# Kernel tuning notes

Measured on AMD Instinct MI355X. Metric: run time of the kernel, lower is better.

## Reference

```python
import jax, jax.numpy as jnp
import numpy as np

B, LAT, H, K = 8, 128, 1024, 294
N, E = 100000, 1600000
XSIZE = 128.0
TAU = 0.5
STEPS = 3


def setup_inputs() -> dict:
    key = jax.random.key(0)
    ks = jax.random.split(key, 20)
    s_in = 1.0 / np.sqrt(LAT)
    s_h = 1.0 / np.sqrt(H)
    inp = {
        "latent": jax.random.normal(ks[0], (B, LAT), jnp.float32),
        "W0": jax.random.normal(ks[1], (LAT, H), jnp.float32) * s_in,
        "b0": jnp.zeros((H,), jnp.float32),
        "W1": jax.random.normal(ks[2], (H, H), jnp.float32) * s_h,
        "b1": jnp.zeros((H,), jnp.float32),
        "W2": jax.random.normal(ks[3], (H, H), jnp.float32) * s_h,
        "b2": jnp.zeros((H,), jnp.float32),
        "W3": jax.random.normal(ks[4], (H, H), jnp.float32) * s_h,
        "b3": jnp.zeros((H,), jnp.float32),
        # coefficient heads use normal(1e-4) init in the source
        "Wx": jax.random.normal(ks[5], (H, K), jnp.float32) * 1e-4,
        "bx": jnp.zeros((K,), jnp.float32),
        "Wy": jax.random.normal(ks[6], (H, K), jnp.float32) * 1e-4,
        "by": jnp.zeros((K,), jnp.float32),
        "Wz": jax.random.normal(ks[7], (H, K), jnp.float32) * 1e-4,
        "bz": jnp.zeros((K,), jnp.float32),
        # precomputed Zernike/spherical basis evaluated at the N coords: [K, N]
        "Z": jax.random.normal(ks[8], (K, N), jnp.float32),
        "edge_weights": jax.random.uniform(ks[9], (E,), jnp.float32),
        "edge_index": jax.random.randint(ks[10], (2, E), 0, N, jnp.int64),
    }
    return inp


def _decode_coefficients(latent, W0, b0, W1, b1, W2, b2, W3, b3,
                         Wx, bx, Wy, by, Wz, bz):
    h = jax.nn.relu(latent @ W0 + b0)
    for W, b in ((W1, b1), (W2, b2), (W3, b3)):
        h = jax.nn.relu(h + h @ W + b)  # residual MLP block
    return h @ Wx + bx, h @ Wy + by, h @ Wz + bz  # [B, K] each


def _diffuse(flow, edge_index, edge_weights):
    """Graph diffusion smoothing of per-node vectors. flow: [B, N, 3]."""
    src, dst = edge_index[0], edge_index[1]
    deg = jax.ops.segment_sum(edge_weights, dst, num_segments=N)
    deg = jnp.maximum(deg, 1e-6)[:, None, None]  # [N,1,1]
    f = jnp.transpose(flow, (1, 0, 2))  # [N, B, 3]
    w = edge_weights[:, None, None]
    for _ in range(STEPS):
        msg = f[src] * w                                        # gather  [E,B,3]
        agg = jax.ops.segment_sum(msg, dst, num_segments=N)     # scatter [N,B,3]
        f = (1.0 - TAU) * f + TAU * agg / deg
    return jnp.transpose(f, (1, 0, 2))  # [B, N, 3]


def reference(latent, W0, b0, W1, b1, W2, b2, W3, b3,
              Wx, bx, Wy, by, Wz, bz, Z, edge_weights, edge_index):
    cx, cy, cz = _decode_coefficients(latent, W0, b0, W1, b1, W2, b2, W3, b3,
                                      Wx, bx, Wy, by, Wz, bz)
    # basis evaluation: per-axis coefficients contracted with Zernike basis
    dx = jnp.einsum("bk,kn->bn", cx, Z)
    dy = jnp.einsum("bk,kn->bn", cy, Z)
    dz = jnp.einsum("bk,kn->bn", cz, Z)
    flow = (0.5 * XSIZE) * jnp.stack([dx, dy, dz], axis=-1)  # [B, N, 3]
    flow = _diffuse(flow, edge_index, edge_weights)
    reg = 1e-4 * jnp.sqrt(jnp.sum(cx ** 2 + cy ** 2 + cz ** 2))
    return flow, reg
```

## Files before the change

### kernel.cpp

```cpp
#include <hip/hip_runtime.h>
#include <math.h>

#define BB 8
#define LAT 128
#define HH 1024
#define KK 294
#define NN 100000
#define EE 1600000
#define NSTEPS 3
#define XS_HALF 64.0f

#define NB 391
#define CS 8
#define COB 28
#define COB2 30
#define EPT 8
#define EST 200000
#define EBLK 782
#define GON 40

#define F2NB 782
#define KPAD 320
#define GS 80

__constant__ float ccoefT[KPAD * 24];


__device__ __forceinline__ void mlp_part_body(int bid, const float* __restrict__ hin,
                                              const float* __restrict__ W,
                                              float* __restrict__ part, int jdim) {
    int it = bid & 15;
    int bs = bid >> 4;
    int tx = threadIdx.x;
    int il = tx & 63;
    int jg = tx >> 6;
    int i = it * 64 + il;
    int j0 = bs * 64;

    __shared__ float hs[8 * 64];
    for (int u = tx; u < 512; u += 256) {
        int b = u >> 6, lj = u & 63;
        hs[u] = hin[b * jdim + j0 + lj];
    }
    __syncthreads();

    float acc[8];
#pragma unroll
    for (int b = 0; b < 8; ++b) acc[b] = 0.0f;
#pragma unroll
    for (int jj = 0; jj < 16; ++jj) {
        int lj = jg * 16 + jj;
        float w = W[(size_t)(j0 + lj) * HH + i];
#pragma unroll
        for (int b = 0; b < 8; ++b) acc[b] += hs[b * 64 + lj] * w;
    }

    __shared__ float red[4][8][64];
#pragma unroll
    for (int b = 0; b < 8; ++b) red[jg][b][il] = acc[b];
    __syncthreads();
    for (int u = tx; u < 512; u += 256) {
        int b = u >> 6, ii = u & 63;
        float s = red[0][b][ii] + red[1][b][ii] + red[2][b][ii] + red[3][b][ii];
        part[(size_t)bs * 8192 + b * HH + it * 64 + ii] = s;
    }
}

__device__ __forceinline__ void mlp_comb_body(int bid, const float* __restrict__ part,
                                              int nsplit, const float* __restrict__ resid,
                                              const float* __restrict__ bias,
                                              float* __restrict__ hout) {
    int idx = bid * 256 + threadIdx.x;
    if (idx >= BB * HH) return;
    int i = idx & (HH - 1);
    float s = bias[i];
    if (resid) s += resid[idx];
    for (int bs = 0; bs < nsplit; ++bs) s += part[(size_t)bs * 8192 + idx];
    hout[idx] = fmaxf(s, 0.0f);
}

__device__ __forceinline__ void count_body(int bid, const int* __restrict__ ei,
                                           int* __restrict__ cnt, int* __restrict__ rank) {
    int gid = bid * 256 + threadIdx.x;
    if (gid >= EST) return;
    int d[EPT];
#pragma unroll
    for (int j = 0; j < EPT; ++j) d[j] = ei[EE + gid + j * EST];
#pragma unroll
    for (int j = 0; j < EPT; ++j) {
        int p = atomicAdd(&cnt[d[j]], 1);
        rank[gid + j * EST] = p;
    }
}

__device__ __forceinline__ void bsum_body(int bid, const int* __restrict__ cnt,
                                          int* __restrict__ bsum) {
    __shared__ int red[256];
    int i = bid * 256 + threadIdx.x;
    red[threadIdx.x] = (i < NN) ? cnt[i] : 0;
    __syncthreads();
    for (int off = 128; off > 0; off >>= 1) {
        if ((int)threadIdx.x < off) red[threadIdx.x] += red[threadIdx.x + off];
        __syncthreads();
    }
    if (threadIdx.x == 0) bsum[bid] = red[0];
}

__device__ __forceinline__ void bscan_body(const int* __restrict__ bsum,
                                           int* __restrict__ bpre,
                                           int* __restrict__ offs) {
    __shared__ int A[512], Bf[512];
    int t = threadIdx.x;
    A[t] = (t < NB) ? bsum[t] : 0;
    A[t + 256] = (t + 256 < NB) ? bsum[t + 256] : 0;
    __syncthreads();
    int* s = A;
    int* d = Bf;
    for (int off = 1; off < 512; off <<= 1) {
        d[t] = s[t] + ((t >= off) ? s[t - off] : 0);
        int u = t + 256;
        d[u] = s[u] + ((u >= off) ? s[u - off] : 0);
        __syncthreads();
        int* tmp = s; s = d; d = tmp;
    }
    if (t < NB) bpre[t] = (t == 0) ? 0 : s[t - 1];
    int u = t + 256;
    if (u < NB) bpre[u] = s[u - 1];
    if (t == 0) offs[NN] = s[NB - 1];
}

__device__ __forceinline__ void offs_body(int bid, const int* __restrict__ cnt,
                                          const int* __restrict__ bpre,
                                          int* __restrict__ offs) {
    __shared__ int part[256];
    int t = threadIdx.x;
    int i = bid * 256 + t;
    int v = (i < NN) ? cnt[i] : 0;
    part[t] = v;
    __syncthreads();
    for (int off = 1; off < 256; off <<= 1) {
        int u = (t >= off) ? part[t - off] : 0;
        __syncthreads();
        part[t] += u;
        __syncthreads();
    }
    if (i < NN) offs[i] = bpre[bid] + part[t] - v;
}

__device__ __forceinline__ void fill_body(int bid, const int* __restrict__ ei,
                                          const float* __restrict__ ew,
                                          const int* __restrict__ offs,
                                          const int* __restrict__ rank,
                                          int2* __restrict__ csr) {
    int gid = bid * 256 + threadIdx.x;
    if (gid >= EST) return;
    int s[EPT], d[EPT], r[EPT];
    float w[EPT];
#pragma unroll
    for (int j = 0; j < EPT; ++j) {
        int e = gid + j * EST;
        s[j] = ei[e];
        d[j] = ei[EE + e];
        w[j] = ew[e];
        r[j] = rank[e];
    }
#pragma unroll
    for (int j = 0; j < EPT; ++j) {
        int p = offs[d[j]] + r[j];
        int2 v;
        v.x = s[j];
        v.y = __float_as_int(w[j]);
        csr[p] = v;
    }
}

__device__ __forceinline__ void degcsr_body(int bid, const int* __restrict__ offs,
                                            const int2* __restrict__ csr,
                                            float* __restrict__ invh) {
    int n = bid * 256 + threadIdx.x;
    if (n >= NN) return;
    int beg = offs[n], end = offs[n + 1];
    float s = 0.0f;
    for (int i = beg; i < end; ++i) s += __int_as_float(csr[i].y);
    invh[n] = 0.5f / fmaxf(s, 1e-6f);
}

__device__ __forceinline__ void flow2_body(int bid, const float* __restrict__ Z,
                                           float* __restrict__ fout) {
    __shared__ float smem[9600];

    int t = threadIdx.x;
    int lane = t & 63;
    int g = t >> 6;
    int gu = __builtin_amdgcn_readfirstlane(g);
    int kb = gu * GS;

    int n0 = bid * 128;
    int np = n0 + 2 * lane;
    bool valid = (np + 1) < NN;
    int npl = valid ? np : (NN - 2);
    const float* zbase = Z + npl;

    float2 acc[24];
#pragma unroll
    for (int j = 0; j < 24; ++j) acc[j] = make_float2(0.f, 0.f);

    float2 zb[8];
#pragma unroll
    for (int d = 0; d < 8; ++d)
        zb[d] = *(const float2*)(zbase + (size_t)((kb + d) * NN));

    for (int c = 0; c < GS / 8; ++c) {
        int base = kb + c * 8;
#pragma unroll
        for (int d = 0; d < 8; ++d) {
            int k = base + d;
            int knl = k + 8;
            if (knl > KK - 1) knl = KK - 1;
            float2 zn = *(const float2*)(zbase + (size_t)knl * NN);
            const float* cf = &ccoefT[k * 24];
#pragma unroll
            for (int j = 0; j < 24; ++j) {
                acc[j].x = fmaf(cf[j], zb[d].x, acc[j].x);
                acc[j].y = fmaf(cf[j], zb[d].y, acc[j].y);
            }
            zb[d] = zn;
        }
    }

    __syncthreads();
    if (g > 0) {
        float2* d = (float2*)(smem + ((g - 1) * 64 + lane) * 50);
#pragma unroll
        for (int j = 0; j < 24; ++j) d[j] = acc[j];
    }
    __syncthreads();
    if (g == 0 && valid) {
#pragma unroll
        for (int s = 0; s < 3; ++s) {
            const float2* r = (const float2*)(smem + (s * 64 + lane) * 50);
#pragma unroll
            for (int j = 0; j < 24; ++j) {
                float2 v = r[j];
                acc[j].x += v.x;
                acc[j].y += v.y;
            }
        }
        float buf[48];
#pragma unroll
        for (int j = 0; j < 24; ++j) {
            buf[j] = XS_HALF * acc[j].x;
            buf[24 + j] = XS_HALF * acc[j].y;
        }
        float4* fr = (float4*)(fout + (size_t)np * 24);
#pragma unroll
        for (int q = 0; q < 12; ++q) fr[q] = ((const float4*)buf)[q];
    }
}

__device__ __forceinline__ void reg_body(const float* __restrict__ coef,
                                         float* __restrict__ out_reg) {
    __shared__ float red[256];
    float s = 0.0f;
    for (int i = threadIdx.x; i < 3 * BB * KK; i += 256) {
        float v = coef[i];
        s += v * v;
    }
    red[threadIdx.x] = s;
    __syncthreads();
    for (int off = 128; off > 0; off >>= 1) {
        if ((int)threadIdx.x < off) red[threadIdx.x] += red[threadIdx.x + off];
        __syncthreads();
    }
    if (threadIdx.x == 0) out_reg[0] = 1e-4f * sqrtf(red[0]);
}


__global__ void K1_mlp0_count(const float* __restrict__ latent, const float* __restrict__ W0,
                              float* __restrict__ part, const int* __restrict__ ei,
                              int* __restrict__ cnt, int* __restrict__ rank) {
    if (blockIdx.x < 32) mlp_part_body(blockIdx.x, latent, W0, part, LAT);
    else count_body(blockIdx.x - 32, ei, cnt, rank);
}

__global__ void K2_comb0_bsum(const float* __restrict__ part, const float* __restrict__ b0,
                              float* __restrict__ hout, const int* __restrict__ cnt,
                              int* __restrict__ bsum) {
    if (blockIdx.x < 32) mlp_comb_body(blockIdx.x, part, 2, nullptr, b0, hout);
    else bsum_body(blockIdx.x - 32, cnt, bsum);
}

__global__ void K3_bscan_mlp1(const int* __restrict__ bsum, int* __restrict__ bpre,
                              int* __restrict__ offs, const float* __restrict__ hin,
                              const float* __restrict__ W1, float* __restrict__ part) {
    if (blockIdx.x == 0) bscan_body(bsum, bpre, offs);
    else mlp_part_body(blockIdx.x - 1, hin, W1, part, HH);
}

__global__ void K4_comb1_offs(const float* __restrict__ part, const float* __restrict__ resid,
                              const float* __restrict__ b1, float* __restrict__ hout,
                              const int* __restrict__ cnt, const int* __restrict__ bpre,
                              int* __restrict__ offs) {
    if (blockIdx.x < 32) mlp_comb_body(blockIdx.x, part, 16, resid, b1, hout);
    else offs_body(blockIdx.x - 32, cnt, bpre, offs);
}

__global__ void K5_mlp2_fill(const float* __restrict__ hin, const float* __restrict__ W2,
                             float* __restrict__ part, const int* __restrict__ ei,
                             const float* __restrict__ ew, const int* __restrict__ offs,
                             const int* __restrict__ rank, int2* __restrict__ csr) {
    if (blockIdx.x < 256) mlp_part_body(blockIdx.x, hin, W2, part, HH);
    else fill_body(blockIdx.x - 256, ei, ew, offs, rank, csr);
}

__global__ void K6_comb2_deg(const float* __restrict__ part, const float* __restrict__ resid,
                             const float* __restrict__ bias, float* __restrict__ hout,
                             const int* __restrict__ offs, const int2* __restrict__ csr,
                             float* __restrict__ invh) {
    if (blockIdx.x < 32) mlp_comb_body(blockIdx.x, part, 16, resid, bias, hout);
    else degcsr_body(blockIdx.x - 32, offs, csr, invh);
}

__global__ void K_mlp_part3(const float* __restrict__ hin, const float* __restrict__ W,
                            float* __restrict__ part) {
    mlp_part_body(blockIdx.x, hin, W, part, HH);
}

__global__ void K_mlp_comb(const float* __restrict__ part, const float* __restrict__ resid,
                           const float* __restrict__ bias, float* __restrict__ hout) {
    mlp_comb_body(blockIdx.x, part, 16, resid, bias, hout);
}

__global__ void k_coef_part(const float* __restrict__ h,
                            const float* __restrict__ Wx,
                            const float* __restrict__ Wy,
                            const float* __restrict__ Wz,
                            float* __restrict__ cpart) {
    int s = blockIdx.x / COB;
    int blk = blockIdx.x % COB;
    int o = blk * 256 + threadIdx.x;
    if (o >= 3 * BB * KK) return;
    int t = o / (BB * KK);
    int r = o % (BB * KK);
    int b = r / KK, k = r % KK;
    const float* W = (t == 0) ? Wx : ((t == 1) ? Wy : Wz);
    const float* hr = h + b * HH;
    int j0 = s * 128;
    float acc = 0.0f;
#pragma unroll 8
    for (int j = 0; j < 128; ++j) acc += hr[j0 + j] * W[(size_t)(j0 + j) * KK + k];
    cpart[(size_t)s * 7056 + o] = acc;
}

__global__ void k_coef_comb(const float* __restrict__ cpart,
                            const float* __restrict__ bx,
                            const float* __restrict__ by,
                            const float* __restrict__ bz,
                            float* __restrict__ coefT) {
    int o = blockIdx.x * 256 + threadIdx.x;
    if (o >= KPAD * 24) return;
    if (o >= 3 * BB * KK) {
        coefT[o] = 0.0f;
        return;
    }
    int t = o / (BB * KK);
    int r = o % (BB * KK);
    int b = r / KK;
    int k = r % KK;
    float s = ((t == 0) ? bx : ((t == 1) ? by : bz))[k];
#pragma unroll
    for (int i = 0; i < CS; ++i) s += cpart[(size_t)i * 7056 + o];
    coefT[k * 24 + b * 3 + t] = s;
}

__global__ void __launch_bounds__(256, 4)
K11_flow_reg(const float* __restrict__ coefT, const float* __restrict__ Z,
             float* __restrict__ fout, float* __restrict__ out_reg) {
    if (blockIdx.x < F2NB) flow2_body(blockIdx.x, Z, fout);
    else reg_body(coefT, out_reg);
}

__global__ void k_gather(const int* __restrict__ offs, const int2* __restrict__ csr,
                         const float* __restrict__ invh,
                         const float* __restrict__ fin, float* __restrict__ fout) {
    int idx = blockIdx.x * 256 + threadIdx.x;
    if (idx >= NN * 6) return;
    int n = idx / 6;
    int q = idx - n * 6;
    int beg = offs[n], end = offs[n + 1];
    const float4* f4 = (const float4*)fin;
    float4 acc = make_float4(0.f, 0.f, 0.f, 0.f);
    if (beg < end) {
        int2 e = csr[beg];
        for (int i = beg; i < end; ++i) {
            int2 en = (i + 1 < end) ? csr[i + 1] : e;
            float w = __int_as_float(e.y);
            float4 fv = f4[(size_t)e.x * 6 + q];
            acc.x += w * fv.x;
            acc.y += w * fv.y;
            acc.z += w * fv.z;
            acc.w += w * fv.w;
            e = en;
        }
    }
    float inv = invh[n];
    float4 fo = f4[(size_t)n * 6 + q];
    float4 r;
    r.x = 0.5f * fo.x + inv * acc.x;
    r.y = 0.5f * fo.y + inv * acc.y;
    r.z = 0.5f * fo.z + inv * acc.z;
    r.w = 0.5f * fo.w + inv * acc.w;
    ((float4*)fout)[(size_t)n * 6 + q] = r;
}

__global__ void k_gather_out(const int* __restrict__ offs, const int2* __restrict__ csr,
                             const float* __restrict__ invh,
                             const float* __restrict__ fin, float* __restrict__ out) {
    __shared__ float ls[GON * 24];
    int t = threadIdx.x;
    int n0 = blockIdx.x * GON;
    if (t < GON * 6) {
        int ln = t / 6, q = t - 6 * ln;
        int n = n0 + ln;
        if (n < NN) {
            int beg = offs[n], end = offs[n + 1];
            const float4* f4 = (const float4*)fin;
            float4 acc = make_float4(0.f, 0.f, 0.f, 0.f);
            if (beg < end) {
                int2 e = csr[beg];
                for (int i = beg; i < end; ++i) {
                    int2 en = (i + 1 < end) ? csr[i + 1] : e;
                    float w = __int_as_float(e.y);
                    float4 fv = f4[(size_t)e.x * 6 + q];
                    acc.x += w * fv.x;
                    acc.y += w * fv.y;
                    acc.z += w * fv.z;
                    acc.w += w * fv.w;
                    e = en;
                }
            }
            float inv = invh[n];
            float4 fo = f4[(size_t)n * 6 + q];
            float* d = &ls[ln * 24 + q * 4];
            d[0] = 0.5f * fo.x + inv * acc.x;
            d[1] = 0.5f * fo.y + inv * acc.y;
            d[2] = 0.5f * fo.z + inv * acc.z;
            d[3] = 0.5f * fo.w + inv * acc.w;
        }
    }
    __syncthreads();
    int cnt = NN - n0; if (cnt > GON) cnt = GON;
    int per_b = cnt * 3;
    for (int b = 0; b < BB; ++b) {
        for (int u = t; u < per_b; u += 256) {
            int n = u / 3;
            int c = u - 3 * n;
            out[(size_t)b * (NN * 3) + (size_t)n0 * 3 + u] = ls[n * 24 + b * 3 + c];
        }
    }
}

extern "C" void kernel_launch(void* const* d_in, const int* in_sizes, int n_in,
                              void* d_out, int out_size, void* d_ws, size_t ws_size,
                              hipStream_t stream) {
    const float* latent = (const float*)d_in[0];
    const float* W0 = (const float*)d_in[1];
    const float* b0 = (const float*)d_in[2];
    const float* W1 = (const float*)d_in[3];
    const float* b1 = (const float*)d_in[4];
    const float* W2 = (const float*)d_in[5];
    const float* b2 = (const float*)d_in[6];
    const float* W3 = (const float*)d_in[7];
    const float* b3 = (const float*)d_in[8];
    const float* Wx = (const float*)d_in[9];
    const float* bx = (const float*)d_in[10];
    const float* Wy = (const float*)d_in[11];
    const float* by = (const float*)d_in[12];
    const float* Wz = (const float*)d_in[13];
    const float* bz = (const float*)d_in[14];
    const float* Z  = (const float*)d_in[15];
    const float* ew = (const float*)d_in[16];
    const int*   ei = (const int*)d_in[17];
    float* out = (float*)d_out;

    float* p = (float*)d_ws;
    float* h_a     = p; p += 8192;
    float* h_b     = p; p += 8192;
    float* hp      = p; p += 16 * 8192;
    float* coef    = p; p += KPAD * 24;
    float* cpart   = p; p += CS * 7056;
    float* invh    = p; p += 100000;
    int*   cnt     = (int*)p; p += 100000;
    int*   offs    = (int*)p; p += 100016;
    int*   bsum    = (int*)p; p += 512;
    int*   bpre    = (int*)p; p += 512;
    int*   rank    = (int*)p; p += 1600000;
    int2*  csr     = (int2*)p; p += 2 * 1600000;
    float* fpart   = p; p += (size_t)2 * NN * 24;

    hipMemsetAsync(cnt, 0, NN * sizeof(int), stream);

    K1_mlp0_count<<<32 + EBLK, 256, 0, stream>>>(latent, W0, hp, ei, cnt, rank);
    K2_comb0_bsum<<<32 + NB, 256, 0, stream>>>(hp, b0, h_a, cnt, bsum);
    K3_bscan_mlp1<<<1 + 256, 256, 0, stream>>>(bsum, bpre, offs, h_a, W1, hp);
    K4_comb1_offs<<<32 + NB, 256, 0, stream>>>(hp, h_a, b1, h_b, cnt, bpre, offs);
    K5_mlp2_fill<<<256 + EBLK, 256, 0, stream>>>(h_b, W2, hp, ei, ew, offs, rank, csr);
    K6_comb2_deg<<<32 + NB, 256, 0, stream>>>(hp, h_b, b2, h_a, offs, csr, invh);
    K_mlp_part3<<<256, 256, 0, stream>>>(h_a, W3, hp);
    K_mlp_comb<<<32, 256, 0, stream>>>(hp, h_a, b3, h_b);
    k_coef_part<<<COB * CS, 256, 0, stream>>>(h_b, Wx, Wy, Wz, cpart);
    k_coef_comb<<<COB2, 256, 0, stream>>>(cpart, bx, by, bz, coef);
    hipMemcpyToSymbolAsync(HIP_SYMBOL(ccoefT), coef, KPAD * 24 * sizeof(float), 0,
                           hipMemcpyDeviceToDevice, stream);
    K11_flow_reg<<<F2NB + 1, 256, 0, stream>>>(coef, Z, fpart, out + (size_t)BB * NN * 3);

    float* f0 = fpart;
    float* f1 = fpart + (size_t)NN * 24;
    k_gather<<<(NN * 6 + 255) / 256, 256, 0, stream>>>(offs, csr, invh, f0, f1);
    k_gather<<<(NN * 6 + 255) / 256, 256, 0, stream>>>(offs, csr, invh, f1, f0);
    k_gather_out<<<(NN + GON - 1) / GON, 256, 0, stream>>>(offs, csr, invh, f0, out);
}
```

Measured before the change: 540.3 us.

## Stream Zernike basis via async global-to-LDS loads and pad atomic counters

Rewrites the basis-contraction kernel so each lane handles one node over all K rows, streaming Z rows into a 4-deep per-wave LDS ring with asynchronous global_load_lds and explicit vmcnt waits instead of register prefetch plus a cross-wave K-split reduction. This removes the shared-memory reduction and is meant to hide memory latency while halving the block count. Separately, the per-node edge counters are spread to a stride of 4 ints to reduce atomic contention in the degree count. The inline-asm wait count and ring reuse rely on careful in-order behaviour and use more LDS and memset work.

```diff
diff --git a/kernel.cpp b/kernel.cpp
--- a/kernel.cpp
+++ b/kernel.cpp
@@ -19,9 +19,8 @@
 #define EBLK 782
 #define GON 40
 
-#define F2NB 782
+#define F3NB 391
 #define KPAD 320
-#define GS 80
 
 __constant__ float ccoefT[KPAD * 24];
 
@@ -88,7 +87,7 @@
     for (int j = 0; j < EPT; ++j) d[j] = ei[EE + gid + j * EST];
 #pragma unroll
     for (int j = 0; j < EPT; ++j) {
-        int p = atomicAdd(&cnt[d[j]], 1);
+        int p = atomicAdd(&cnt[d[j] * 4], 1);
         rank[gid + j * EST] = p;
     }
 }
@@ -97,7 +96,7 @@
                                           int* __restrict__ bsum) {
     __shared__ int red[256];
     int i = bid * 256 + threadIdx.x;
-    red[threadIdx.x] = (i < NN) ? cnt[i] : 0;
+    red[threadIdx.x] = (i < NN) ? cnt[i * 4] : 0;
     __syncthreads();
     for (int off = 128; off > 0; off >>= 1) {
         if ((int)threadIdx.x < off) red[threadIdx.x] += red[threadIdx.x + off];
@@ -135,7 +134,7 @@
     __shared__ int part[256];
     int t = threadIdx.x;
     int i = bid * 256 + t;
-    int v = (i < NN) ? cnt[i] : 0;
+    int v = (i < NN) ? cnt[i * 4] : 0;
     part[t] = v;
     __syncthreads();
     for (int off = 1; off < 256; off <<= 1) {
@@ -185,76 +184,59 @@
     invh[n] = 0.5f / fmaxf(s, 1e-6f);
 }
 
-__device__ __forceinline__ void flow2_body(int bid, const float* __restrict__ Z,
+__device__ __forceinline__ void flow3_body(int bid, const float* __restrict__ Z,
                                            float* __restrict__ fout) {
-    __shared__ float smem[9600];
+    __shared__ float zl[4][4][8][64];
 
     int t = threadIdx.x;
     int lane = t & 63;
-    int g = t >> 6;
-    int gu = __builtin_amdgcn_readfirstlane(g);
-    int kb = gu * GS;
-
-    int n0 = bid * 128;
-    int np = n0 + 2 * lane;
-    bool valid = (np + 1) < NN;
-    int npl = valid ? np : (NN - 2);
-    const float* zbase = Z + npl;
-
-    float2 acc[24];
-#pragma unroll
-    for (int j = 0; j < 24; ++j) acc[j] = make_float2(0.f, 0.f);
-
-    float2 zb[8];
-#pragma unroll
-    for (int d = 0; d < 8; ++d)
-        zb[d] = *(const float2*)(zbase + (size_t)((kb + d) * NN));
-
-    for (int c = 0; c < GS / 8; ++c) {
-        int base = kb + c * 8;
+    int wu = __builtin_amdgcn_readfirstlane(t >> 6);
+
+    int n = bid * 256 + (wu << 6) + lane;
+    int nn = (n < NN) ? n : (NN - 1);
+    const float* zn = Z + nn;
+
+    float acc[24];
+#pragma unroll
+    for (int j = 0; j < 24; ++j) acc[j] = 0.0f;
+
+    auto issue = [&](int cp) {
+        int b = cp & 3;
 #pragma unroll
         for (int d = 0; d < 8; ++d) {
-            int k = base + d;
-            int knl = k + 8;
-            if (knl > KK - 1) knl = KK - 1;
-            float2 zn = *(const float2*)(zbase + (size_t)knl * NN);
-            const float* cf = &ccoefT[k * 24];
-#pragma unroll
-            for (int j = 0; j < 24; ++j) {
-                acc[j].x = fmaf(cf[j], zb[d].x, acc[j].x);
-                acc[j].y = fmaf(cf[j], zb[d].y, acc[j].y);
-            }
-            zb[d] = zn;
+            int r = cp * 8 + d;
+            int rz = (r < KK) ? r : (KK - 1);
+            __builtin_amdgcn_global_load_lds(
+                (__attribute__((address_space(1))) unsigned int*)(zn + (size_t)rz * NN),
+                (__attribute__((address_space(3))) unsigned int*)(&zl[wu][b][d][0]),
+                4, 0, 0);
         }
-    }
-
-    __syncthreads();
-    if (g > 0) {
-        float2* d = (float2*)(smem + ((g - 1) * 64 + lane) * 50);
-#pragma unroll
-        for (int j = 0; j < 24; ++j) d[j] = acc[j];
-    }
-    __syncthreads();
-    if (g == 0 && valid) {
-#pragma unroll
-        for (int s = 0; s < 3; ++s) {
-            const float2* r = (const float2*)(smem + (s * 64 + lane) * 50);
-#pragma unroll
-            for (int j = 0; j < 24; ++j) {
-                float2 v = r[j];
-                acc[j].x += v.x;
-                acc[j].y += v.y;
-            }
+    };
+
+    issue(0); issue(1); issue(2);
+
+#pragma unroll 1
+    for (int c = 0; c < 37; ++c) {
+        issue(c + 3);
+        asm volatile("s_waitcnt vmcnt(24)" ::: "memory");
+        __builtin_amdgcn_sched_barrier(0);
+        int b = c & 3;
+#pragma unroll
+        for (int d = 0; d < 8; ++d) {
+            float z = zl[wu][b][d][lane];
+            const float* cf = &ccoefT[(c * 8 + d) * 24];
+#pragma unroll
+            for (int j = 0; j < 24; ++j) acc[j] = fmaf(cf[j], z, acc[j]);
         }
-        float buf[48];
-#pragma unroll
-        for (int j = 0; j < 24; ++j) {
-            buf[j] = XS_HALF * acc[j].x;
-            buf[24 + j] = XS_HALF * acc[j].y;
-        }
-        float4* fr = (float4*)(fout + (size_t)np * 24);
-#pragma unroll
-        for (int q = 0; q < 12; ++q) fr[q] = ((const float4*)buf)[q];
+    }
+
+    if (n < NN) {
+        float buf4[24];
+#pragma unroll
+        for (int j = 0; j < 24; ++j) buf4[j] = XS_HALF * acc[j];
+        float4* fr = (float4*)(fout + (size_t)n * 24);
+#pragma unroll
+        for (int q = 0; q < 6; ++q) fr[q] = ((const float4*)buf4)[q];
     }
 }
 
@@ -373,10 +355,9 @@
     coefT[k * 24 + b * 3 + t] = s;
 }
 
-__global__ void __launch_bounds__(256, 4)
-K11_flow_reg(const float* __restrict__ coefT, const float* __restrict__ Z,
-             float* __restrict__ fout, float* __restrict__ out_reg) {
-    if (blockIdx.x < F2NB) flow2_body(blockIdx.x, Z, fout);
+__global__ void K11_flow_reg(const float* __restrict__ coefT, const float* __restrict__ Z,
+                             float* __restrict__ fout, float* __restrict__ out_reg) {
+    if (blockIdx.x < F3NB) flow3_body(blockIdx.x, Z, fout);
     else reg_body(coefT, out_reg);
 }
 
@@ -490,7 +471,7 @@
     float* coef    = p; p += KPAD * 24;
     float* cpart   = p; p += CS * 7056;
     float* invh    = p; p += 100000;
-    int*   cnt     = (int*)p; p += 100000;
+    int*   cnt     = (int*)p; p += 400000;
     int*   offs    = (int*)p; p += 100016;
     int*   bsum    = (int*)p; p += 512;
     int*   bpre    = (int*)p; p += 512;
@@ -498,7 +479,7 @@
     int2*  csr     = (int2*)p; p += 2 * 1600000;
     float* fpart   = p; p += (size_t)2 * NN * 24;
 
-    hipMemsetAsync(cnt, 0, NN * sizeof(int), stream);
+    hipMemsetAsync(cnt, 0, 400000 * sizeof(int), stream);
 
     K1_mlp0_count<<<32 + EBLK, 256, 0, stream>>>(latent, W0, hp, ei, cnt, rank);
     K2_comb0_bsum<<<32 + NB, 256, 0, stream>>>(hp, b0, h_a, cnt, bsum);
@@ -512,7 +493,7 @@
     k_coef_comb<<<COB2, 256, 0, stream>>>(cpart, bx, by, bz, coef);
     hipMemcpyToSymbolAsync(HIP_SYMBOL(ccoefT), coef, KPAD * 24 * sizeof(float), 0,
                            hipMemcpyDeviceToDevice, stream);
-    K11_flow_reg<<<F2NB + 1, 256, 0, stream>>>(coef, Z, fpart, out + (size_t)BB * NN * 3);
+    K11_flow_reg<<<F3NB + 1, 256, 0, stream>>>(coef, Z, fpart, out + (size_t)BB * NN * 3);
 
     float* f0 = fpart;
     float* f1 = fpart + (size_t)NN * 24;
```

Result: no change. 536.5 us (-0.7%).
